# Optimization experiments

Measured on AMD Instinct MI355X. Metric: run time of the kernel, lower is better.

## Reference

```python
import jax, jax.numpy as jnp
import numpy as np


def setup_inputs() -> dict:
    key = jax.random.key(0)
    k1, k2, k3, k4, k5 = jax.random.split(key, 5)
    B, A, FI = 4096, 256, 16   # batch, atoms, iso functions per atom
    Bo, FA = 512, 8            # bonds, aniso functions per bond
    return {
        "c_iso": jax.random.normal(k1, (B, A, FI), dtype=jnp.float32),
        "c_aniso": jax.random.normal(k2, (B, Bo, FA), dtype=jnp.float32),
        "int_iso": jax.random.uniform(k3, (B, A, FI), dtype=jnp.float32),
        "int_aniso": jax.random.uniform(k4, (B, Bo, FA), dtype=jnp.float32),
        "charge": jax.random.normal(k5, (B, A), dtype=jnp.float32),
    }


def reference(c_iso, c_aniso, int_iso, int_aniso, charge):
    # Bordered KKT system from the Lagrangian L(x,u) = (x-c)^T(x-c) - u (q^T x - Q):
    #   q^T x     = Q
    # Exact closed-form solution (Sherman-Morrison on the rank-1 border):
    #   u = 2 (Q - q^T c) / (q^T q),   x = c + (u/2) q
    B = c_iso.shape[0]
    c = jnp.concatenate([c_iso.reshape(B, -1), c_aniso.reshape(B, -1)], axis=1)   # [B, n]
    q = jnp.concatenate([int_iso.reshape(B, -1), int_aniso.reshape(B, -1)], axis=1)  # [B, n]
    Q = jnp.sum(charge, axis=1)                                                   # [B]
    qTc = jnp.einsum("bn,bn->b", q, c)
    qTq = jnp.einsum("bn,bn->b", q, q)
    u = 2.0 * (Q - qTc) / qTq                                                     # Lagrange multiplier [B]
    x = c + 0.5 * u[:, None] * q                                                  # [B, n]
    n_iso = c_iso.shape[1] * c_iso.shape[2]
    sol_iso = x[:, :n_iso].reshape(c_iso.shape)
    sol_aniso = x[:, n_iso:].reshape(c_aniso.shape)
    return (sol_iso, sol_aniso)
```

## Files before the change

kernel.cpp:

```cpp
#include <hip/hip_runtime.h>


#define HALF_N 4096
#define BLOCK  256
#define WPB    4

typedef float v4f __attribute__((ext_vector_type(4)));

__global__ __launch_bounds__(BLOCK, 4) void qp_charge_norm_kernel(
    const float* __restrict__ c_iso,
    const float* __restrict__ c_aniso,
    const float* __restrict__ q_iso,
    const float* __restrict__ q_aniso,
    const float* __restrict__ charge,
    float* __restrict__ out,
    int B)
{
    const int tid  = threadIdx.x;
    const int lane = tid & 63;
    const int wave = tid >> 6;
    const int b    = blockIdx.x * WPB + wave;

    const v4f* ci = (const v4f*)(c_iso   + (size_t)b * HALF_N);
    const v4f* ca = (const v4f*)(c_aniso + (size_t)b * HALF_N);
    const v4f* qi = (const v4f*)(q_iso   + (size_t)b * HALF_N);
    const v4f* qa = (const v4f*)(q_aniso + (size_t)b * HALF_N);

    float qc = 0.0f, qq = 0.0f;
#pragma unroll
    for (int j = 0; j < 16; ++j) {
        const int idx = j * 64 + lane;
        v4f cvi = ci[idx], qvi = qi[idx];
        v4f cva = ca[idx], qva = qa[idx];
        qc += qvi.x * cvi.x + qvi.y * cvi.y + qvi.z * cvi.z + qvi.w * cvi.w;
        qq += qvi.x * qvi.x + qvi.y * qvi.y + qvi.z * qvi.z + qvi.w * qvi.w;
        qc += qva.x * cva.x + qva.y * cva.y + qva.z * cva.z + qva.w * cva.w;
        qq += qva.x * qva.x + qva.y * qva.y + qva.z * qva.z + qva.w * qva.w;
    }
    v4f chv = ((const v4f*)(charge + (size_t)b * 256))[lane];
    float Qp = chv.x + chv.y + chv.z + chv.w;

#pragma unroll
    for (int off = 32; off > 0; off >>= 1) {
        qc += __shfl_down(qc, off, 64);
        qq += __shfl_down(qq, off, 64);
        Qp += __shfl_down(Qp, off, 64);
    }
    const float h = __shfl((Qp - qc) / qq, 0, 64);

    v4f* oi = (v4f*)(out + (size_t)b * HALF_N);
    v4f* oa = (v4f*)(out + (size_t)B * HALF_N + (size_t)b * HALF_N);
#pragma unroll
    for (int j = 0; j < 16; ++j) {
        const int idx = j * 64 + lane;
        v4f r = ci[idx] + h * qi[idx];
        __builtin_nontemporal_store(r, &oi[idx]);
        v4f s = ca[idx] + h * qa[idx];
        __builtin_nontemporal_store(s, &oa[idx]);
    }
}

extern "C" void kernel_launch(void* const* d_in, const int* in_sizes, int n_in,
                              void* d_out, int out_size, void* d_ws, size_t ws_size,
                              hipStream_t stream) {
    const float* c_iso   = (const float*)d_in[0];
    const float* c_aniso = (const float*)d_in[1];
    const float* q_iso   = (const float*)d_in[2];
    const float* q_aniso = (const float*)d_in[3];
    const float* charge  = (const float*)d_in[4];
    float* out = (float*)d_out;

    const int B = in_sizes[0] / HALF_N;

    qp_charge_norm_kernel<<<B / WPB, BLOCK, 0, stream>>>(
        c_iso, c_aniso, q_iso, q_aniso, charge, out, B);
}
```

Before: 372.0 us.

## Stage each row in LDS via direct global-to-LDS loads, one block per row

Each block now owns one batch row and copies the row's c and q data into shared memory with global_load_lds DMA. Both the dot-product reduction and the output pass then read from LDS. This removes the second global read of the inputs. A cross-wave reduction through shared memory is added, and the 64KB of LDS per block limits how many blocks fit on a CU.

```diff
diff --git a/kernel.cpp b/kernel.cpp
--- a/kernel.cpp
+++ b/kernel.cpp
@@ -2,10 +2,17 @@
 
 
 #define HALF_N 4096
-#define BLOCK  256
-#define WPB    4
+#define BLOCK  512
+#define NWAVE  (BLOCK / 64)
 
 typedef float v4f __attribute__((ext_vector_type(4)));
+
+__device__ __forceinline__ void dma16(const float* g, float* l) {
+    __builtin_amdgcn_global_load_lds(
+        (const __attribute__((address_space(1))) float*)g,
+        (__attribute__((address_space(3))) float*)l,
+        16, 0, 0);
+}
 
 __global__ __launch_bounds__(BLOCK, 4) void qp_charge_norm_kernel(
     const float* __restrict__ c_iso,
@@ -16,46 +23,68 @@
     float* __restrict__ out,
     int B)
 {
+    __shared__ float sc[2 * HALF_N];
+    __shared__ float sq[2 * HALF_N];
+    __shared__ float s_qc[NWAVE], s_qq[NWAVE], s_Q[NWAVE];
+
     const int tid  = threadIdx.x;
     const int lane = tid & 63;
     const int wave = tid >> 6;
-    const int b    = blockIdx.x * WPB + wave;
+    const int b    = blockIdx.x;
 
-    const v4f* ci = (const v4f*)(c_iso   + (size_t)b * HALF_N);
-    const v4f* ca = (const v4f*)(c_aniso + (size_t)b * HALF_N);
-    const v4f* qi = (const v4f*)(q_iso   + (size_t)b * HALF_N);
-    const v4f* qa = (const v4f*)(q_aniso + (size_t)b * HALF_N);
+    const float* ci = c_iso   + (size_t)b * HALF_N;
+    const float* ca = c_aniso + (size_t)b * HALF_N;
+    const float* qi = q_iso   + (size_t)b * HALF_N;
+    const float* qa = q_aniso + (size_t)b * HALF_N;
 
+#pragma unroll
+    for (int t = 0; t < 2; ++t) {
+        const int k   = wave * 2 + t;
+        const int off = k * 256;
+        const int gl  = off + lane * 4;
+        dma16(ci + gl, sc + off);
+        dma16(ca + gl, sc + HALF_N + off);
+        dma16(qi + gl, sq + off);
+        dma16(qa + gl, sq + HALF_N + off);
+    }
+    float Qp = (tid < 256) ? charge[(size_t)b * 256 + tid] : 0.0f;
+
+    __syncthreads();
+
+    const v4f* sc4 = (const v4f*)sc;
+    const v4f* sq4 = (const v4f*)sq;
     float qc = 0.0f, qq = 0.0f;
 #pragma unroll
-    for (int j = 0; j < 16; ++j) {
-        const int idx = j * 64 + lane;
-        v4f cvi = ci[idx], qvi = qi[idx];
-        v4f cva = ca[idx], qva = qa[idx];
-        qc += qvi.x * cvi.x + qvi.y * cvi.y + qvi.z * cvi.z + qvi.w * cvi.w;
-        qq += qvi.x * qvi.x + qvi.y * qvi.y + qvi.z * qvi.z + qvi.w * qvi.w;
-        qc += qva.x * cva.x + qva.y * cva.y + qva.z * cva.z + qva.w * cva.w;
-        qq += qva.x * qva.x + qva.y * qva.y + qva.z * qva.z + qva.w * qva.w;
+    for (int j = 0; j < 4; ++j) {
+        const int idx = j * BLOCK + tid;
+        v4f cv = sc4[idx];
+        v4f qv = sq4[idx];
+        qc += qv.x * cv.x + qv.y * cv.y + qv.z * cv.z + qv.w * cv.w;
+        qq += qv.x * qv.x + qv.y * qv.y + qv.z * qv.z + qv.w * qv.w;
     }
-    v4f chv = ((const v4f*)(charge + (size_t)b * 256))[lane];
-    float Qp = chv.x + chv.y + chv.z + chv.w;
-
 #pragma unroll
     for (int off = 32; off > 0; off >>= 1) {
         qc += __shfl_down(qc, off, 64);
         qq += __shfl_down(qq, off, 64);
         Qp += __shfl_down(Qp, off, 64);
     }
-    const float h = __shfl((Qp - qc) / qq, 0, 64);
+    if (lane == 0) { s_qc[wave] = qc; s_qq[wave] = qq; s_Q[wave] = Qp; }
+    __syncthreads();
+
+    float tqc = 0.0f, tqq = 0.0f, tQ = 0.0f;
+#pragma unroll
+    for (int w = 0; w < NWAVE; ++w) { tqc += s_qc[w]; tqq += s_qq[w]; tQ += s_Q[w]; }
+    const float h = (tQ - tqc) / tqq;
 
     v4f* oi = (v4f*)(out + (size_t)b * HALF_N);
     v4f* oa = (v4f*)(out + (size_t)B * HALF_N + (size_t)b * HALF_N);
 #pragma unroll
-    for (int j = 0; j < 16; ++j) {
-        const int idx = j * 64 + lane;
-        v4f r = ci[idx] + h * qi[idx];
+    for (int j = 0; j < 2; ++j) {
+        const int idx = j * BLOCK + tid;
+        v4f r = sc4[idx] + h * sq4[idx];
         __builtin_nontemporal_store(r, &oi[idx]);
-        v4f s = ca[idx] + h * qa[idx];
+        const int idxA = idx + HALF_N / 4;
+        v4f s = sc4[idxA] + h * sq4[idxA];
         __builtin_nontemporal_store(s, &oa[idx]);
     }
 }
@@ -72,6 +101,6 @@
 
     const int B = in_sizes[0] / HALF_N;
 
-    qp_charge_norm_kernel<<<B / WPB, BLOCK, 0, stream>>>(
+    qp_charge_norm_kernel<<<B, BLOCK, 0, stream>>>(
         c_iso, c_aniso, q_iso, q_aniso, charge, out, B);
 }
```

Measured after the change: 329.5 us. 11.4% less time.
